# Kernel tuning notes

Measured on AMD Instinct MI355X. Metric: run time of the kernel, lower is better.

The kernel has to match this reference:

```python
import jax, jax.numpy as jnp
import numpy as np

B = 32
SEQ_LEN = 512      # T and n_fft
PRED_LEN = 96      # STFT window_size = PRED_LEN // 2 = 48
TOP_K = 3
D_MODEL = 512
D_FF = 512
N_HEADS = 8
C_OUT = 32         # graph node count
NODE_DIM = 10
CONV_CH = 32
SKIP_CH = 32
GCN_DEPTH = 2
PROP_ALPHA = 0.05
HOP = 48
EPS = 1e-5


def layer_norm(x, g, b):
    m = x.mean(-1, keepdims=True)
    v = ((x - m) ** 2).mean(-1, keepdims=True)
    return (x - m) * jax.lax.rsqrt(v + EPS) * g + b


def stft_mag(x):
    """torch.stft(center=True, hann window of len 48 center-padded to n_fft) magnitude,
    vmapped over channels. Returns [B, frames, n_fft//2+1, N]."""
    n_fft = SEQ_LEN
    win_len = PRED_LEN // 2
    n = jnp.arange(win_len, dtype=x.dtype)
    win = 0.5 - 0.5 * jnp.cos(2.0 * jnp.pi * n / win_len)   # periodic hann
    pad_l = (n_fft - win_len) // 2
    win = jnp.pad(win, (pad_l, n_fft - win_len - pad_l))     # center-pad window to n_fft
    T = x.shape[1]
    xp = jnp.pad(x, ((0, 0), (n_fft // 2, n_fft // 2), (0, 0)), mode='reflect')
    nfr = T // HOP + 1
    idx = jnp.arange(nfr)[:, None] * HOP + jnp.arange(n_fft)[None, :]
    frames = xp[:, idx, :]                                   # [B, nfr, n_fft, N]
    spec = jnp.fft.rfft(frames * win[None, None, :, None], axis=2)
    return jnp.abs(spec)


def attention_block(x, wq, bq, wk, bk, wv, bv, wo, bo, ff1_w, ff1_b, ff2_w, ff2_b,
                    n1_g, n1_b, n2_g, n2_b):
    M, S, D = x.shape
    H, Dh = N_HEADS, D // N_HEADS
    q = (x @ wq.T + bq).reshape(M, S, H, Dh)
    k = (x @ wk.T + bk).reshape(M, S, H, Dh)
    v = (x @ wv.T + bv).reshape(M, S, H, Dh)
    scores = jnp.einsum('mshd,mthd->mhst', q, k) * (1.0 / float(np.sqrt(Dh)))
    o = jnp.einsum('mhst,mthd->mshd', jax.nn.softmax(scores, axis=-1), v).reshape(M, S, D)
    x1 = layer_norm(x + (o @ wo.T + bo), n1_g, n1_b)
    y = jax.nn.gelu(x1 @ ff1_w.T + ff1_b, approximate=False) @ ff2_w.T + ff2_b
    return layer_norm(x1 + y, n2_g, n2_b)


def graph_block(x, nv1, nv2, sw, sb, mw, mb, ew, eb, lw, lb, g, b):
    # adaptive adjacency over C_OUT nodes
    adp = jax.nn.softmax(jax.nn.relu(nv1 @ nv2), axis=1)
    adj = adp + jnp.eye(C_OUT, dtype=x.dtype)
    a = adj / adj.sum(1, keepdims=True)
    # start_conv: [B,1,D,T] -> [B,CONV_CH,C_OUT,T]
    h = jax.lax.conv_general_dilated(x.transpose(0, 2, 1)[:, None], sw, (1, 1), 'VALID',
                                     dimension_numbers=('NCHW', 'OIHW', 'NCHW'))
    h = h + sb[None, :, None, None]
    x0, outs = h, [h]
    for _ in range(GCN_DEPTH):  # mixprop
        h = PROP_ALPHA * x0 + (1.0 - PROP_ALPHA) * jnp.einsum('bcwt,vw->bcvt', h, a)
        outs.append(h)
    ho = jnp.einsum('oc,bcnt->bont', mw, jnp.concatenate(outs, axis=1)) + mb[None, :, None, None]
    h = jax.nn.gelu(ho, approximate=False)
    out = jnp.einsum('bcns,tcs->btn', h, ew) + eb[None, :, None]   # end_conv (1,seq_len) kernel
    out = out @ lw + lb                                            # Linear c_out -> d_model
    return layer_norm(x + out, g, b)


def setup_inputs() -> dict:
    ks = jax.random.split(jax.random.key(0), 32)
    r = lambda i, shape, s=0.02: jax.random.normal(ks[i], shape, jnp.float32) * s
    kh = D_MODEL - C_OUT + 1
    return {
        'x': jax.random.normal(ks[0], (B, SEQ_LEN, D_MODEL), jnp.float32),
        'nv1': r(1, (TOP_K, C_OUT, NODE_DIM), 1.0),
        'nv2': r(2, (TOP_K, NODE_DIM, C_OUT), 1.0),
        'start_w': r(3, (TOP_K, CONV_CH, 1, kh, 1)),
        'start_b': r(4, (TOP_K, CONV_CH)),
        'mix_w': r(5, (TOP_K, SKIP_CH, (GCN_DEPTH + 1) * CONV_CH)),
        'mix_b': r(6, (TOP_K, SKIP_CH)),
        'end_w': r(7, (TOP_K, SEQ_LEN, SKIP_CH, SEQ_LEN)),
        'end_b': r(8, (TOP_K, SEQ_LEN)),
        'glin_w': r(9, (TOP_K, C_OUT, D_MODEL)),
        'glin_b': r(10, (TOP_K, D_MODEL)),
        'gnorm_g': 1.0 + r(11, (TOP_K, D_MODEL), 0.1),
        'gnorm_b': r(12, (TOP_K, D_MODEL), 0.1),
        'wq': r(13, (D_MODEL, D_MODEL)), 'bq': r(14, (D_MODEL,)),
        'wk': r(15, (D_MODEL, D_MODEL)), 'bk': r(16, (D_MODEL,)),
        'wv': r(17, (D_MODEL, D_MODEL)), 'bv': r(18, (D_MODEL,)),
        'wo': r(19, (D_MODEL, D_MODEL)), 'bo': r(20, (D_MODEL,)),
        'ff1_w': r(21, (D_FF, D_MODEL)), 'ff1_b': r(22, (D_FF,)),
        'ff2_w': r(23, (D_MODEL, D_FF)), 'ff2_b': r(24, (D_MODEL,)),
        'an1_g': 1.0 + r(25, (D_MODEL,), 0.1), 'an1_b': r(26, (D_MODEL,), 0.1),
        'an2_g': 1.0 + r(27, (D_MODEL,), 0.1), 'an2_b': r(28, (D_MODEL,), 0.1),
        'norm_g': 1.0 + r(29, (D_MODEL,), 0.1), 'norm_b': r(30, (D_MODEL,), 0.1),
    }


def reference(x, nv1, nv2, start_w, start_b, mix_w, mix_b, end_w, end_b, glin_w, glin_b,
              gnorm_g, gnorm_b, wq, bq, wk, bk, wv, bv, wo, bo,
              ff1_w, ff1_b, ff2_w, ff2_b, an1_g, an1_b, an2_g, an2_b, norm_g, norm_b):
    Bx, T, N = x.shape
    mag = stft_mag(x)                                   # [B, frames, Fbins, N]
    freq = mag.mean(axis=(0, 1, 3)).at[0].set(0.0)
    top = np.asarray(jax.lax.top_k(freq, TOP_K)[1])     # concrete: shapes below are data-dependent
    periods = [int(T // int(f)) for f in top]
    sw = jax.nn.softmax(mag[:, :, top, :].mean(axis=(1, 3)), axis=1)  # [B, k] scale weights
    cur = x
    res = []
    for i in range(TOP_K):
        scale = periods[i]
        # NOTE: faithful to the original bug: x is overwritten by gconv output each iteration
        cur = graph_block(cur, nv1[i], nv2[i], start_w[i], start_b[i], mix_w[i], mix_b[i],
                          end_w[i], end_b[i], glin_w[i], glin_b[i], gnorm_g[i], gnorm_b[i])
        length = -(-T // scale) * scale
        out = jnp.pad(cur, ((0, 0), (0, length - T), (0, 0))) if length > T else cur
        out = out.reshape(Bx * (length // scale), scale, N)
        out = attention_block(out, wq, bq, wk, bk, wv, bv, wo, bo,
                              ff1_w, ff1_b, ff2_w, ff2_b, an1_g, an1_b, an2_g, an2_b)
        out = jax.nn.gelu(layer_norm(out, norm_g, norm_b), approximate=False)
        out = out.reshape(Bx, length, N)[:, :T]
        res.append(out)
    res = jnp.stack(res, axis=-1)                       # [B, T, N, k]
    return (res * sw[:, None, None, :]).sum(-1) + cur
```

## Files before the change

### kernel.cpp

```cpp
#include <hip/hip_runtime.h>
#include <math.h>

#define DI __device__ __forceinline__

namespace {
constexpr int B_ = 32;
constexpr int T_ = 512;
constexpr int N_ = 512;
constexpr int C_ = 32;
constexpr int KH_ = 481;
constexpr int HOP_ = 48;
constexpr int WIN_ = 48;
constexpr int NFR_ = 11;
constexpr int NBIN_ = 257;
constexpr int NSB_ = 8 * NFR_ * B_;
constexpr int TOKMAX = 21760;
constexpr int PLW = TOKMAX * 512;
constexpr float EPS_ = 1e-5f;

constexpr size_t MBY = 1ull << 20;
constexpr size_t OFF_META = 0;
constexpr size_t OFF_FREQ = 4096;
constexpr size_t OFF_SW   = 8192;
constexpr size_t OFF_BEFF = 16384;
constexpr size_t OFF_P12  = 32768;
constexpr size_t OFF_FSB  = 65536;
constexpr size_t OFF_OSM  = 1 * MBY;
constexpr size_t OFF_WB   = 4 * MBY;
constexpr size_t OFF_WDH  = 10 * MBY;
constexpr size_t OFF_EWH  = 12 * MBY;
constexpr size_t OFF_CUR  = 44 * MBY;
constexpr size_t OFF_ACC  = 76 * MBY;
constexpr size_t TR       = 108 * MBY;
constexpr size_t OFF_T    = TR;
constexpr size_t OFF_WPH  = TR + 6 * MBY;
constexpr size_t OFF_G    = TR + 64 * MBY;
constexpr size_t OFF_G2   = TR + 128 * MBY;
constexpr size_t OFF_PART = TR + 192 * MBY;
constexpr size_t OFF_A0 = TR;
constexpr size_t OFF_A2 = TR + 44 * MBY;
constexpr size_t OFF_A3 = TR + 88 * MBY;
constexpr size_t OFF_A4 = TR + 132 * MBY;
constexpr size_t OFF_A5 = TR + 176 * MBY;
constexpr size_t OFF_FP = TR;
}

typedef __attribute__((ext_vector_type(2))) float f32x2;
typedef __attribute__((ext_vector_type(4))) float f32x4;
typedef __attribute__((ext_vector_type(8))) short bf8;
typedef __attribute__((ext_vector_type(8))) unsigned short u16x8;

DI float gelu_exact(float x) { return 0.5f * x * (1.0f + erff(x * 0.7071067811865475f)); }
DI unsigned short f2bf(float f) {
  unsigned u = __float_as_uint(f);
  u += 0x7FFFu + ((u >> 16) & 1u);
  return (unsigned short)(u >> 16);
}
DI float bf2f(unsigned short s) { return __uint_as_float(((unsigned)s) << 16); }
DI float ld2(const unsigned short* __restrict__ H, const unsigned short* __restrict__ L,
             size_t i) { return bf2f(H[i]) + bf2f(L[i]); }
DI void st2(unsigned short* __restrict__ H, unsigned short* __restrict__ L,
            size_t i, float v) {
  unsigned short h = f2bf(v);
  H[i] = h;
  L[i] = f2bf(v - bf2f(h));
}
DI void gll16(const unsigned short* g, unsigned short* l) {
  __builtin_amdgcn_global_load_lds(
      (const __attribute__((address_space(1))) void*)g,
      (__attribute__((address_space(3))) void*)l, 16, 0, 0);
}

__global__ __launch_bounds__(256) void k_stft2(const float* __restrict__ x,
                                               float* __restrict__ fpart) {
  int bid = blockIdx.x;
  int cc = bid & 7;
  int f = (bid >> 3) % NFR_;
  int b = bid / (8 * NFR_);
  __shared__ float xw[WIN_][64];
  int tid = threadIdx.x;
  for (int i = tid; i < WIN_ * 64; i += 256) {
    int j = i >> 6, n = i & 63;
    int gi = f * HOP_ + 232 + j - 256;
    if (gi < 0) gi = -gi;
    float w = 0.5f - 0.5f * cosf((float)j * 0.13089969389957472f);
    xw[j][n] = w * x[((size_t)b * T_ + gi) * N_ + cc * 64 + n];
  }
  __syncthreads();
  for (int pair = tid; pair < NBIN_ * 8; pair += 256) {
    int k = pair >> 3;
    int c4 = (pair & 7) * 4;
    int r0 = (k * 232) & 511;
    float a0 = (float)r0 * 0.012271846303085130f;
    float c = cosf(a0), s = sinf(a0);
    float dA = (float)k * 0.012271846303085130f;
    float cd = cosf(dA), sd = sinf(dA);
    f32x2 ri[8];
#pragma unroll
    for (int q = 0; q < 8; ++q) ri[q] = (f32x2){0.f, 0.f};
#pragma unroll 4
    for (int j = 0; j < WIN_; ++j) {
      float4 v0 = *(const float4*)&xw[j][c4];
      float4 v1 = *(const float4*)&xw[j][32 + c4];
      f32x2 cs = (f32x2){c, s};
      ri[0] += v0.x * cs;
      ri[1] += v0.y * cs;
      ri[2] += v0.z * cs;
      ri[3] += v0.w * cs;
      ri[4] += v1.x * cs;
      ri[5] += v1.y * cs;
      ri[6] += v1.z * cs;
      ri[7] += v1.w * cs;
      float cn = c * cd - s * sd;
      s = s * cd + c * sd;
      c = cn;
    }
    float m = 0.f;
#pragma unroll
    for (int q = 0; q < 8; ++q) m += sqrtf(ri[q].x * ri[q].x + ri[q].y * ri[q].y);
    for (int off = 4; off > 0; off >>= 1) m += __shfl_xor(m, off);
    if ((tid & 7) == 0) fpart[(size_t)k * NSB_ + bid] = m;
  }
}

__global__ __launch_bounds__(256) void k_fred(const float* __restrict__ fpart,
                                              float* __restrict__ freq,
                                              float* __restrict__ fsumb) {
  int k = blockIdx.x;
  int tid = threadIdx.x;
  int b = tid >> 3, j = tid & 7;
  float s = 0.f;
  for (int i = j; i < 88; i += 8) s += fpart[(size_t)k * NSB_ + b * 88 + i];
  for (int off = 4; off > 0; off >>= 1) s += __shfl_xor(s, off);
  __shared__ float bs[32];
  if (j == 0) bs[b] = s;
  __syncthreads();
  if (tid < 32) {
    float v = bs[tid];
    fsumb[k * 32 + tid] = v;
    for (int off = 16; off > 0; off >>= 1) v += __shfl_xor(v, off);
    if (tid == 0) freq[k] = v;
  }
}

__global__ void k_topk(const float* __restrict__ freq, const float* __restrict__ fsumb,
                       int* __restrict__ meta, float* __restrict__ swb) {
  __shared__ int stop[3];
  int tid = threadIdx.x;
  if (tid == 0) {
    float bv[3] = {-1e30f, -1e30f, -1e30f};
    int bi[3] = {1, 1, 1};
    for (int k = 1; k < NBIN_; ++k) {
      float v = freq[k];
      if (v > bv[0]) { bv[2]=bv[1]; bi[2]=bi[1]; bv[1]=bv[0]; bi[1]=bi[0]; bv[0]=v; bi[0]=k; }
      else if (v > bv[1]) { bv[2]=bv[1]; bi[2]=bi[1]; bv[1]=v; bi[1]=k; }
      else if (v > bv[2]) { bv[2]=v; bi[2]=k; }
    }
    for (int i = 0; i < 3; ++i) {
      int top = bi[i];
      int p = T_ / top;
      int L = ((T_ + p - 1) / p) * p;
      meta[i] = top;
      meta[3 + i] = p;
      meta[6 + i] = L;
      meta[9 + i] = L / p;
      meta[15 + i] = B_ * L;
      stop[i] = top;
    }
  }
  __syncthreads();
  int b = tid;
  if (b < B_) {
    float inv = 1.0f / (float)(NFR_ * N_);
    float m0 = fsumb[stop[0] * 32 + b] * inv;
    float m1 = fsumb[stop[1] * 32 + b] * inv;
    float m2 = fsumb[stop[2] * 32 + b] * inv;
    float mx = fmaxf(m0, fmaxf(m1, m2));
    float e0 = expf(m0 - mx), e1 = expf(m1 - mx), e2 = expf(m2 - mx);
    float s = e0 + e1 + e2;
    swb[b * 4 + 0] = e0 / s; swb[b * 4 + 1] = e1 / s; swb[b * 4 + 2] = e2 / s;
  }
}

__global__ __launch_bounds__(1024) void k_adjprep(const float* __restrict__ nv1,
                                                  const float* __restrict__ nv2,
                                                  const float* __restrict__ mw,
                                                  const float* __restrict__ mb,
                                                  const float* __restrict__ sb,
                                                  float* __restrict__ P12,
                                                  float* __restrict__ beff) {
  __shared__ float A32s[32][32];
  __shared__ float Ms[32][32], P1s[32][32], P2s[32][32], S1[32], S2[32], sbl[32];
  int tid = threadIdx.x;
  if (tid < 32) {
    int v = tid;
    float row[32];
    for (int w = 0; w < 32; ++w) {
      float s = 0.f;
      for (int d = 0; d < 10; ++d) s += nv1[v * 10 + d] * nv2[d * 32 + w];
      row[w] = fmaxf(s, 0.f);
    }
    float mx = -1e30f;
    for (int w = 0; w < 32; ++w) mx = fmaxf(mx, row[w]);
    float sm = 0.f;
    for (int w = 0; w < 32; ++w) { row[w] = expf(row[w] - mx); sm += row[w]; }
    for (int w = 0; w < 32; ++w) row[w] /= sm;
    row[v] += 1.0f;
    float rs = 0.f;
    for (int w = 0; w < 32; ++w) rs += row[w];
    for (int w = 0; w < 32; ++w) A32s[v][w] = row[w] / rs;
    sbl[tid] = sb[tid];
  }
  __syncthreads();
  int w = tid >> 5, v = tid & 31;
  Ms[w][v] = A32s[v][w];
  __syncthreads();
  float p1 = 0.95f * Ms[w][v] + (w == v ? 0.05f : 0.f);
  P1s[w][v] = p1;
  __syncthreads();
  float p2 = 0.f;
  for (int u = 0; u < 32; ++u) p2 += P1s[w][u] * Ms[u][v];
  p2 = 0.95f * p2 + (w == v ? 0.05f : 0.f);
  P2s[w][v] = p2;
  P12[tid] = p1;
  P12[1024 + tid] = p2;
  __syncthreads();
  if (tid < 32) {
    float s1 = 0.f, s2 = 0.f;
    for (int u = 0; u < 32; ++u) { s1 += P1s[u][tid]; s2 += P2s[u][tid]; }
    S1[tid] = s1; S2[tid] = s2;
  }
  __syncthreads();
  int o = w;
  float be = mb[o];
  for (int c = 0; c < 32; ++c) {
    float sc = sbl[c];
    be += mw[o * 96 + c] * sc;
    be += mw[o * 96 + 32 + c] * sc * S1[v];
    be += mw[o * 96 + 64 + c] * sc * S2[v];
  }
  beff[tid] = be;
}

__global__ __launch_bounds__(256) void k_T(const float* __restrict__ P12,
                                           const float* __restrict__ mw,
                                           float* __restrict__ Tm) {
  int idx = blockIdx.x * 256 + threadIdx.x;
  int r = idx >> 10, k2 = idx & 1023;
  int o = r >> 5, v = r & 31;
  int c = k2 >> 5, w = k2 & 31;
  float t = mw[o * 96 + 32 + c] * P12[w * 32 + v]
          + mw[o * 96 + 64 + c] * P12[1024 + w * 32 + v];
  if (w == v) t += mw[o * 96 + c];
  Tm[idx] = t;
}

__global__ void k_wdh(const float* __restrict__ swi, unsigned short* __restrict__ WH) {
  int idx = blockIdx.x * 256 + threadIdx.x;
  int j = idx >> 10, k2 = idx & 1023;
  int c = k2 >> 5, w = k2 & 31;
  int kk = j - w;
  float vv = (kk >= 0 && kk < KH_) ? swi[c * KH_ + kk] : 0.f;
  WH[idx] = f2bf(vv);
}

__global__ void k_splith(const float* __restrict__ src, unsigned short* __restrict__ Hi,
                         int n) {
  int i = blockIdx.x * 256 + threadIdx.x;
  if (i * 4 >= n) return;
  float4 v = *(const float4*)&src[i * 4];
  ushort4 h;
  h.x = f2bf(v.x); h.y = f2bf(v.y); h.z = f2bf(v.z); h.w = f2bf(v.w);
  *(ushort4*)&Hi[i * 4] = h;
}

__global__ __launch_bounds__(256, 2) void k_mm2(
    const float* __restrict__ A, const unsigned short* __restrict__ Bh,
    const float* __restrict__ bias,
    float* __restrict__ C, float* __restrict__ Cpart,
    int M, int N, int K, int lda, int dogelu) {
  const int bm = blockIdx.y * 128;
  if (bm >= M) return;
  const int bn = blockIdx.x * 128;
  const int nz = gridDim.z, z = blockIdx.z;
  const int kpb = K / nz;
  const int kbeg = z * kpb, kend = kbeg + kpb;

  __shared__ __align__(16) unsigned short AhS[4096], AlS[4096], BhS[4096];

  const int tid = threadIdx.x;
  const int wave = tid >> 6, lane = tid & 63;
  const int wr = wave >> 1, wc = wave & 1;
  const int fr = lane & 15, fs = lane >> 4;

  const int sr = tid >> 1, ss = (tid & 1) * 2;
  const int sx = (sr >> 1) & 3;
  const int so0 = sr * 32 + 8 * (ss ^ sx);
  const int so1 = sr * 32 + 8 * ((ss + 1) ^ sx);

  const int row0 = tid >> 2;
  const int s0 = (tid & 3) ^ ((row0 >> 1) & 3);
  const unsigned short* gBh0 = Bh + (size_t)(bn + row0) * K + s0 * 8;
  const unsigned short* gBh1 = gBh0 + (size_t)64 * K;
  unsigned short* lB0 = &BhS[wave * 512];
  unsigned short* lB1 = &BhS[2048 + wave * 512];

  int aoff[4], boff[4];
#pragma unroll
  for (int m = 0; m < 4; ++m) {
    int ra = wr * 64 + m * 16 + fr;
    aoff[m] = ra * 32 + 8 * (fs ^ ((ra >> 1) & 3));
    int rb = wc * 64 + m * 16 + fr;
    boff[m] = rb * 32 + 8 * (fs ^ ((rb >> 1) & 3));
  }

  const bool aok = (bm + sr) < M;
  const float* Arow = A + (size_t)(bm + sr) * lda + ss * 8;

  f32x4 acc[4][4];
#pragma unroll
  for (int m = 0; m < 4; ++m)
#pragma unroll
    for (int n = 0; n < 4; ++n) acc[m][n] = (f32x4){0.f, 0.f, 0.f, 0.f};

  for (int k0 = kbeg; k0 < kend; k0 += 32) {
    float4 a0, a1, a2, a3;
    if (aok) {
      const float4* p = (const float4*)(Arow + k0);
      a0 = p[0]; a1 = p[1]; a2 = p[2]; a3 = p[3];
    } else {
      a0 = a1 = a2 = a3 = make_float4(0.f, 0.f, 0.f, 0.f);
    }
    float av[16];
    av[0]=a0.x; av[1]=a0.y; av[2]=a0.z; av[3]=a0.w;
    av[4]=a1.x; av[5]=a1.y; av[6]=a1.z; av[7]=a1.w;
    av[8]=a2.x; av[9]=a2.y; av[10]=a2.z; av[11]=a2.w;
    av[12]=a3.x; av[13]=a3.y; av[14]=a3.z; av[15]=a3.w;
    u16x8 h0, h1, l0, l1;
#pragma unroll
    for (int j = 0; j < 8; ++j) {
      unsigned u = __float_as_uint(av[j]);
      h0[j] = (unsigned short)(u >> 16);
      float r2 = av[j] - __uint_as_float(u & 0xffff0000u);
      l0[j] = (unsigned short)(__float_as_uint(r2) >> 16);
      unsigned u2 = __float_as_uint(av[j + 8]);
      h1[j] = (unsigned short)(u2 >> 16);
      float r3 = av[j + 8] - __uint_as_float(u2 & 0xffff0000u);
      l1[j] = (unsigned short)(__float_as_uint(r3) >> 16);
    }
    __syncthreads();
    gll16(gBh0 + k0, lB0); gll16(gBh1 + k0, lB1);
    *(u16x8*)&AhS[so0] = h0; *(u16x8*)&AhS[so1] = h1;
    *(u16x8*)&AlS[so0] = l0; *(u16x8*)&AlS[so1] = l1;
    __syncthreads();
    bf8 ah[4], al4[4], bh4[4];
#pragma unroll
    for (int m = 0; m < 4; ++m) {
      ah[m]  = *(const bf8*)&AhS[aoff[m]];
      al4[m] = *(const bf8*)&AlS[aoff[m]];
    }
#pragma unroll
    for (int n = 0; n < 4; ++n) bh4[n] = *(const bf8*)&BhS[boff[n]];
#pragma unroll
    for (int m = 0; m < 4; ++m)
#pragma unroll
      for (int n = 0; n < 4; ++n) {
        acc[m][n] = __builtin_amdgcn_mfma_f32_16x16x32_bf16(ah[m],  bh4[n], acc[m][n], 0, 0, 0);
        acc[m][n] = __builtin_amdgcn_mfma_f32_16x16x32_bf16(al4[m], bh4[n], acc[m][n], 0, 0, 0);
      }
  }

  if (nz > 1) {
    float* P = Cpart + (size_t)z * M * N;
#pragma unroll
    for (int m = 0; m < 4; ++m)
#pragma unroll
      for (int r = 0; r < 4; ++r) {
        int row = bm + wr * 64 + m * 16 + fs * 4 + r;
        if (row < M) {
#pragma unroll
          for (int n = 0; n < 4; ++n) {
            int col = bn + wc * 64 + n * 16 + fr;
            P[(size_t)row * N + col] = acc[m][n][r];
          }
        }
      }
  } else {
    float bcol[4];
#pragma unroll
    for (int n = 0; n < 4; ++n) bcol[n] = bias ? bias[bn + wc * 64 + n * 16 + fr] : 0.f;
#pragma unroll
    for (int m = 0; m < 4; ++m)
#pragma unroll
      for (int r = 0; r < 4; ++r) {
        int row = bm + wr * 64 + m * 16 + fs * 4 + r;
        if (row < M) {
#pragma unroll
          for (int n = 0; n < 4; ++n) {
            int col = bn + wc * 64 + n * 16 + fr;
            float v = acc[m][n][r] + bcol[n];
            if (dogelu) v = gelu_exact(v);
            C[(size_t)row * N + col] = v;
          }
        }
      }
  }
}

__global__ __launch_bounds__(256, 4) void k_mmcv(
    const float* __restrict__ A, const unsigned short* __restrict__ Bh,
    const float* __restrict__ bias,
    unsigned short* __restrict__ C,
    int M, int N, int K, int lda) {
  const int bm = blockIdx.y * 128;
  const int bn = blockIdx.x * 128;

  __shared__ __align__(16) unsigned short AhS[4096], BhS[4096];

  const int tid = threadIdx.x;
  const int wave = tid >> 6, lane = tid & 63;
  const int wr = wave >> 1, wc = wave & 1;
  const int fr = lane & 15, fs = lane >> 4;

  const int sr = tid >> 1, ss = (tid & 1) * 2;
  const int sx = (sr >> 1) & 3;
  const int so0 = sr * 32 + 8 * (ss ^ sx);
  const int so1 = sr * 32 + 8 * ((ss + 1) ^ sx);

  const int row0 = tid >> 2;
  const int s0 = (tid & 3) ^ ((row0 >> 1) & 3);
  const unsigned short* gBh0 = Bh + (size_t)(bn + row0) * K + s0 * 8;
  const unsigned short* gBh1 = gBh0 + (size_t)64 * K;
  unsigned short* lB0 = &BhS[wave * 512];
  unsigned short* lB1 = &BhS[2048 + wave * 512];

// ... 411 lines not shown
  __syncthreads();
  float d0 = val[0] - mean, d1 = val[1] - mean;
  red[tid] = d0 * d0 + d1 * d1;
  __syncthreads();
  for (int off = 128; off > 0; off >>= 1) { if (tid < off) red[tid] += red[tid + off]; __syncthreads(); }
  float inv = rsqrtf(red[0] * (1.0f / N_) + EPS_);
  st2(dh, dl, (size_t)tok * N_ + tid, d0 * inv * g[tid] + bt[tid]);
  st2(dh, dl, (size_t)tok * N_ + tid + 256, d1 * inv * g[tid + 256] + bt[tid + 256]);
}

__global__ __launch_bounds__(256) void k_lnfin(const unsigned short* __restrict__ r1h,
                                               const unsigned short* __restrict__ r1l,
                                               const unsigned short* __restrict__ r2h,
                                               const unsigned short* __restrict__ r2l,
                                               const float* __restrict__ g1,
                                               const float* __restrict__ b1,
                                               const float* __restrict__ g2,
                                               const float* __restrict__ b2,
                                               const float* __restrict__ swb,
                                               float* __restrict__ acc,
                                               const int* __restrict__ meta, int iter) {
  int L = meta[6 + iter];
  int tok = blockIdx.x;
  if (tok >= B_ * L) return;
  int b = tok / L, l = tok % L;
  if (l >= T_) return;
  __shared__ float red[256];
  int tid = threadIdx.x;
  float val[2];
#pragma unroll
  for (int q = 0; q < 2; ++q) {
    size_t i = (size_t)tok * N_ + tid + q * 256;
    val[q] = ld2(r1h, r1l, i) + ld2(r2h, r2l, i);
  }
  red[tid] = val[0] + val[1];
  __syncthreads();
  for (int off = 128; off > 0; off >>= 1) { if (tid < off) red[tid] += red[tid + off]; __syncthreads(); }
  float mean = red[0] * (1.0f / N_);
  __syncthreads();
  float d0 = val[0] - mean, d1 = val[1] - mean;
  red[tid] = d0 * d0 + d1 * d1;
  __syncthreads();
  for (int off = 128; off > 0; off >>= 1) { if (tid < off) red[tid] += red[tid + off]; __syncthreads(); }
  float inv = rsqrtf(red[0] * (1.0f / N_) + EPS_);
  float y0 = d0 * inv * g1[tid] + b1[tid];
  float y1 = d1 * inv * g1[tid + 256] + b1[tid + 256];
  __syncthreads();
  red[tid] = y0 + y1;
  __syncthreads();
  for (int off = 128; off > 0; off >>= 1) { if (tid < off) red[tid] += red[tid + off]; __syncthreads(); }
  float mean2 = red[0] * (1.0f / N_);
  __syncthreads();
  float e0 = y0 - mean2, e1 = y1 - mean2;
  red[tid] = e0 * e0 + e1 * e1;
  __syncthreads();
  for (int off = 128; off > 0; off >>= 1) { if (tid < off) red[tid] += red[tid + off]; __syncthreads(); }
  float inv2 = rsqrtf(red[0] * (1.0f / N_) + EPS_);
  float s = swb[b * 4 + iter];
  float u0 = gelu_exact(e0 * inv2 * g2[tid] + b2[tid]);
  float u1 = gelu_exact(e1 * inv2 * g2[tid + 256] + b2[tid + 256]);
  size_t o = ((size_t)b * T_ + l) * N_;
  acc[o + tid] += s * u0;
  acc[o + tid + 256] += s * u1;
}

__global__ __launch_bounds__(256) void k_attn32(
    const unsigned short* __restrict__ qh,
    const unsigned short* __restrict__ kh,
    const unsigned short* __restrict__ vh,
    unsigned short* __restrict__ oh,
    const int* __restrict__ meta, int iter) {
  int S = meta[3 + iter];
  if (S > 32) return;
  int L = meta[6 + iter], nseq = meta[9 + iter];
  int npair = B_ * nseq * 8;
  __shared__ float Kt[4][64 * 33];
  __shared__ unsigned short Vsh[4][32 * 66];
  __shared__ float qs[4][64];
  int tid = threadIdx.x;
  int wave = tid >> 6, lane = tid & 63;
  float* Ktw = Kt[wave];
  unsigned short* Vw = Vsh[wave];
  int gw = (blockIdx.x * 256 + tid) >> 6;
  int nw = (gridDim.x * 256) >> 6;
  const int tt = lane & 31;
  const int hf = lane >> 5;
  for (int pair = gw; pair < npair; pair += nw) {
    int h = pair & 7;
    int m = pair >> 3;
    int b = m / nseq, g2 = m - b * nseq;
    size_t base = ((size_t)b * L + (size_t)g2 * S) * N_ + h * 64;
    for (int i = lane; i < S * 64; i += 64) {
      int t = i >> 6, d = i & 63;
      size_t gi = base + (size_t)t * N_ + d;
      Ktw[d * 33 + t] = bf2f(kh[gi]);
      Vw[t * 66 + d] = vh[gi];
    }
    bool tok = tt < S;
    for (int s = 0; s < S; ++s) {
      qs[wave][lane] = bf2f(qh[base + (size_t)s * N_ + lane]);
      float part = 0.f;
      if (tok) {
        const float* kp = &Ktw[hf * 32 * 33 + tt];
        const float* qp = &qs[wave][hf * 32];
#pragma unroll 8
        for (int j = 0; j < 32; ++j) part += qp[j] * kp[j * 33];
      }
      part += __shfl_xor(part, 32);
      float sc = tok ? part * 0.125f : -3.0e38f;
      float mx = sc;
      for (int off = 16; off > 0; off >>= 1) mx = fmaxf(mx, __shfl_xor(mx, off));
      float p = tok ? expf(sc - mx) : 0.f;
      float ssum = p;
      for (int off = 16; off > 0; off >>= 1) ssum += __shfl_xor(ssum, off);
      float ov = 0.f;
      for (int t = 0; t < S; ++t) {
        float pt = __shfl(p, t);
        ov += pt * bf2f(Vw[t * 66 + lane]);
      }
      oh[base + (size_t)s * N_ + lane] = f2bf(ov / ssum);
    }
  }
}

__global__ __launch_bounds__(512) void k_attn_small(
    const unsigned short* __restrict__ qh,
    const unsigned short* __restrict__ kh,
    const unsigned short* __restrict__ vh,
    unsigned short* __restrict__ oh,
    const int* __restrict__ meta, int iter) {
  int S = meta[3 + iter];
  if (S <= 32 || S > 128) return;
  int L = meta[6 + iter], nseq = meta[9 + iter];
  int M = B_ * nseq;
  int mh = blockIdx.x;
  int m = mh >> 3, h = mh & 7;
  if (m >= M) return;
  int b = m / nseq, g2 = m % nseq;
  size_t tok0 = (size_t)b * L + (size_t)g2 * S;
  __shared__ float Ks[64 * 129];
  __shared__ float Vs[128 * 65];
  __shared__ float qrow[8][64];
  __shared__ float Pr[8][128];
  int tid = threadIdx.x;
  for (int i = tid; i < S * 64; i += 512) {
    int t = i >> 6, d = i & 63;
    size_t gi = (tok0 + t) * N_ + h * 64 + d;
    Ks[d * 129 + t] = bf2f(kh[gi]);
    Vs[t * 65 + d] = bf2f(vh[gi]);
  }
  __syncthreads();
  int wave = tid >> 6, lane = tid & 63;
  for (int s = wave; s < S; s += 8) {
    qrow[wave][lane] = bf2f(qh[(tok0 + s) * N_ + h * 64 + lane]);
    float sc0 = -3.0e38f, sc1 = -3.0e38f;
    if (lane < S) {
      float ad = 0.f;
#pragma unroll 16
      for (int j = 0; j < 64; ++j) ad += qrow[wave][j] * Ks[j * 129 + lane];
      sc0 = ad * 0.125f;
    }
    if (S > 64 && lane + 64 < S) {
      float ad = 0.f;
#pragma unroll 16
      for (int j = 0; j < 64; ++j) ad += qrow[wave][j] * Ks[j * 129 + lane + 64];
      sc1 = ad * 0.125f;
    }
    float mx = fmaxf(sc0, sc1);
    for (int off = 32; off > 0; off >>= 1) mx = fmaxf(mx, __shfl_xor(mx, off));
    float e0 = (lane < S) ? expf(sc0 - mx) : 0.f;
    float e1 = (S > 64 && lane + 64 < S) ? expf(sc1 - mx) : 0.f;
    if (lane < S) Pr[wave][lane] = e0;
    if (S > 64 && lane + 64 < S) Pr[wave][lane + 64] = e1;
    float ssum = e0 + e1;
    for (int off = 32; off > 0; off >>= 1) ssum += __shfl_xor(ssum, off);
    float ov = 0.f;
#pragma unroll 8
    for (int t = 0; t < S; ++t) ov += Pr[wave][t] * Vs[t * 65 + lane];
    oh[(tok0 + s) * N_ + h * 64 + lane] = f2bf(ov / ssum);
  }
}

__global__ __launch_bounds__(256) void k_attn_big(
    const unsigned short* __restrict__ qh,
    const unsigned short* __restrict__ kh,
    const unsigned short* __restrict__ vh,
    unsigned short* __restrict__ oh,
    const int* __restrict__ meta, int iter) {
  int p = meta[3 + iter];
  if (p <= 128) return;
  int L = meta[6 + iter], nseq = meta[9 + iter];
  int M = B_ * nseq;
  int mh = blockIdx.x;
  int m = mh >> 3, h = mh & 7;
  if (m >= M) return;
  int S = p;
  int b = m / nseq, g2 = m % nseq;
  size_t tok0 = (size_t)b * L + (size_t)g2 * S;
  __shared__ unsigned short Ks[512 * 66];
  __shared__ unsigned short Vs[512 * 66];
  __shared__ float qrow[4][64];
  __shared__ float Pr[4][512];
  int tid = threadIdx.x;
  for (int i = tid; i < S * 64; i += 256) {
    int t = i >> 6, d = i & 63;
    size_t gi = (tok0 + t) * N_ + h * 64 + d;
    Ks[t * 66 + d] = kh[gi];
    Vs[t * 66 + d] = vh[gi];
  }
  __syncthreads();
  int wave = tid >> 6, lane = tid & 63;
  for (int s = wave; s < S; s += 4) {
    qrow[wave][lane] = bf2f(qh[(tok0 + s) * N_ + h * 64 + lane]);
    const float2* qp = (const float2*)&qrow[wave][0];
    float sc[8];
    float mx = -3.0e38f;
#pragma unroll
    for (int c2 = 0; c2 < 8; ++c2) {
      int t = lane + c2 * 64;
      float sv = -3.0e38f;
      if (t < S) {
        const unsigned int* kp = (const unsigned int*)&Ks[t * 66];
        float ad = 0.f;
#pragma unroll
        for (int j2 = 0; j2 < 32; ++j2) {
          float2 qq = qp[j2];
          unsigned int kw = kp[j2];
          ad += qq.x * bf2f((unsigned short)(kw & 0xffffu));
          ad += qq.y * bf2f((unsigned short)(kw >> 16));
        }
        sv = ad * 0.125f;
      }
      sc[c2] = sv;
      mx = fmaxf(mx, sv);
    }
    for (int off = 32; off > 0; off >>= 1) mx = fmaxf(mx, __shfl_xor(mx, off));
    float ssum = 0.f;
#pragma unroll
    for (int c2 = 0; c2 < 8; ++c2) {
      int t = lane + c2 * 64;
      float e = 0.f;
      if (t < S) { e = expf(sc[c2] - mx); Pr[wave][t] = e; }
      ssum += e;
    }
    for (int off = 32; off > 0; off >>= 1) ssum += __shfl_xor(ssum, off);
    float inv = 1.0f / ssum;
    float ov = 0.f;
#pragma unroll 8
    for (int t = 0; t < S; ++t) ov += Pr[wave][t] * bf2f(Vs[t * 66 + lane]);
    oh[(tok0 + s) * N_ + h * 64 + lane] = f2bf(ov * inv);
  }
}

__global__ void k_final(const float* __restrict__ acc, const float* __restrict__ cur,
                        float* __restrict__ out) {
  size_t idx = (size_t)blockIdx.x * 256 + threadIdx.x;
  out[idx] = acc[idx] + cur[idx];
}

extern "C" void kernel_launch(void* const* d_in, const int* in_sizes, int n_in,
                              void* d_out, int out_size, void* d_ws, size_t ws_size,
                              hipStream_t stream) {
  (void)in_sizes; (void)n_in; (void)out_size; (void)ws_size;
  const float* x       = (const float*)d_in[0];
  const float* nv1     = (const float*)d_in[1];
  const float* nv2     = (const float*)d_in[2];
  const float* start_w = (const float*)d_in[3];
  const float* start_b = (const float*)d_in[4];
  const float* mix_w   = (const float*)d_in[5];
  const float* mix_b   = (const float*)d_in[6];
  const float* end_w   = (const float*)d_in[7];
  const float* end_b   = (const float*)d_in[8];
  const float* glin_w  = (const float*)d_in[9];
  const float* glin_b  = (const float*)d_in[10];
  const float* gnorm_g = (const float*)d_in[11];
  const float* gnorm_b = (const float*)d_in[12];
  const float* wq = (const float*)d_in[13];
  const float* bq = (const float*)d_in[14];
  const float* wk = (const float*)d_in[15];
  const float* bk = (const float*)d_in[16];
  const float* wv = (const float*)d_in[17];
  const float* bv = (const float*)d_in[18];
  const float* wo = (const float*)d_in[19];
  const float* bo = (const float*)d_in[20];
  const float* ff1w = (const float*)d_in[21];
  const float* ff1b = (const float*)d_in[22];
  const float* ff2w = (const float*)d_in[23];
  const float* ff2b = (const float*)d_in[24];
  const float* an1g = (const float*)d_in[25];
  const float* an1b = (const float*)d_in[26];
  const float* an2g = (const float*)d_in[27];
  const float* an2b = (const float*)d_in[28];
  const float* nrmg = (const float*)d_in[29];
  const float* nrmb = (const float*)d_in[30];

  char* ws = (char*)d_ws;
  int*   meta = (int*)(ws + OFF_META);
  float* freq = (float*)(ws + OFF_FREQ);
  float* swb  = (float*)(ws + OFF_SW);
  float* beff = (float*)(ws + OFF_BEFF);
  float* P12  = (float*)(ws + OFF_P12);
  float* fsumb = (float*)(ws + OFF_FSB);
  float* osm  = (float*)(ws + OFF_OSM);
  unsigned short* WB  = (unsigned short*)(ws + OFF_WB);
  unsigned short* WdH = (unsigned short*)(ws + OFF_WDH);
  unsigned short* EWH = (unsigned short*)(ws + OFF_EWH);
  float* cur  = (float*)(ws + OFF_CUR);
  float* accb = (float*)(ws + OFF_ACC);
  float* fpart = (float*)(ws + OFF_FP);
  float* Tm   = (float*)(ws + OFF_T);
  unsigned short* WPH = (unsigned short*)(ws + OFF_WPH);
  unsigned short* Gb  = (unsigned short*)(ws + OFF_G);
  unsigned short* G2b = (unsigned short*)(ws + OFF_G2);
  float* PART = (float*)(ws + OFF_PART);
  unsigned short* A0h = (unsigned short*)(ws + OFF_A0); unsigned short* A0l = A0h + PLW;
  unsigned short* A2h = (unsigned short*)(ws + OFF_A2); unsigned short* A2l = A2h + PLW;
  unsigned short* A3h = (unsigned short*)(ws + OFF_A3); unsigned short* A3l = A3h + PLW;
  unsigned short* A4h = (unsigned short*)(ws + OFF_A4);
  unsigned short* A5h = (unsigned short*)(ws + OFF_A5); unsigned short* A5l = A5h + PLW;

  hipMemsetAsync(accb, 0, (size_t)B_ * T_ * N_ * 4, stream);

  k_stft2<<<NSB_, 256, 0, stream>>>(x, fpart);
  k_fred<<<NBIN_, 256, 0, stream>>>(fpart, freq, fsumb);
  k_topk<<<1, 64, 0, stream>>>(freq, fsumb, meta, swb);

  const float* wlist[6] = {wq, wk, wv, wo, ff1w, ff2w};
  for (int w = 0; w < 6; ++w)
    k_splith<<<256, 256, 0, stream>>>(wlist[w], WB + (size_t)w * 262144, 262144);
  unsigned short* WqkvH = WB;
  unsigned short* WoH = WB + 3 * 262144;
  unsigned short* F1H = WB + 4 * 262144;
  unsigned short* F2H = WB + 5 * 262144;

  const float* curIn = x;
  for (int i = 0; i < 3; ++i) {
    k_adjprep<<<1, 1024, 0, stream>>>(nv1 + i * C_ * 10, nv2 + i * 10 * C_,
                                      mix_w + i * C_ * 96, mix_b + i * C_,
                                      start_b + i * C_, P12, beff);
    k_T<<<4096, 256, 0, stream>>>(P12, mix_w + i * C_ * 96, Tm);
    k_wdh<<<2048, 256, 0, stream>>>(start_w + i * C_ * KH_, WdH);
    k_mm2<<<dim3(4, 8, 8), 256, 0, stream>>>(Tm, WdH, nullptr, nullptr, PART,
                                             1024, 512, 1024, 1024, 0);
    k_redsplit<<<2048, 256, 0, stream>>>(PART, WPH);
    k_mmcv<<<dim3(8, 128), 256, 0, stream>>>(curIn, WPH, beff, Gb, 16384, 1024, 512, 512);
    k_repackb<<<B_ * C_ * 16, 256, 0, stream>>>(Gb, G2b);
    k_splith<<<8192, 256, 0, stream>>>(end_w + (size_t)i * 8388608, EWH, 8388608);
    k_mmend<<<dim3(4, 8, 16), 256, 0, stream>>>(G2b, EWH, PART, 1024, 512, 16384);
    k_red16<<<2048, 256, 0, stream>>>(PART, end_b + i * T_, osm);
    k_lwln<<<B_ * T_, 256, 0, stream>>>(osm, glin_w + i * C_ * N_, glin_b + i * N_, curIn,
                                        gnorm_g + i * N_, gnorm_b + i * N_, cur,
                                        A0h, A0l, meta, i);
    k_padtail<<<512, 256, 0, stream>>>(A0h, A0l, meta, i);
    const int* Mdyn = meta + 15 + i;
    dim3 gT(4, TOKMAX / 128, 1);
    k_mmqkv<<<dim3(12, TOKMAX / 128), 256, 0, stream>>>(A0h, WqkvH, bq, bk, bv,
                                                        A2h, A3h, A4h, TOKMAX, 512, Mdyn);
    k_attn32<<<2048, 256, 0, stream>>>(A2h, A3h, A4h, A5h, meta, i);
    k_attn_small<<<4096, 512, 0, stream>>>(A2h, A3h, A4h, A5h, meta, i);
    k_attn_big<<<1024, 256, 0, stream>>>(A2h, A3h, A4h, A5h, meta, i);
    k_mmb1<<<gT, 256, 0, stream>>>(A5h, WoH, bo, A2h, A2l, TOKMAX, 512, 512, Mdyn, 0);
    k_lnadd<<<TOKMAX, 256, 0, stream>>>(A0h, A0l, A2h, A2l, an1g, an1b, A3h, A3l, meta, i);
    k_mmb1<<<gT, 256, 0, stream>>>(A3h, F1H, ff1b, A4h, nullptr, TOKMAX, 512, 512, Mdyn, 1);
    k_mmb1<<<gT, 256, 0, stream>>>(A4h, F2H, ff2b, A5h, A5l, TOKMAX, 512, 512, Mdyn, 0);
    k_lnfin<<<TOKMAX, 256, 0, stream>>>(A3h, A3l, A5h, A5l, an2g, an2b, nrmg, nrmb,
                                        swb, accb, meta, i);
    curIn = cur;
  }
  k_final<<<(B_ * T_ * N_) / 256, 256, 0, stream>>>(accb, curIn, (float*)d_out);
}
```

Measured before the change: 2.016 ms.

## Recast STFT magnitude as split-bf16 MFMA GEMM against precomputed twiddles

```diff
diff --git a/kernel.cpp b/kernel.cpp
--- a/kernel.cpp
+++ b/kernel.cpp
@@ -13,7 +13,7 @@
 constexpr int WIN_ = 48;
 constexpr int NFR_ = 11;
 constexpr int NBIN_ = 257;
-constexpr int NSB_ = 8 * NFR_ * B_;
+constexpr int NMT_ = B_ * NFR_ * 4;
 constexpr int TOKMAX = 21760;
 constexpr int PLW = TOKMAX * 512;
 constexpr float EPS_ = 1e-5f;
@@ -26,6 +26,8 @@
 constexpr size_t OFF_P12  = 32768;
 constexpr size_t OFF_FSB  = 65536;
 constexpr size_t OFF_OSM  = 1 * MBY;
+constexpr size_t OFF_TWH  = 3 * MBY;
+constexpr size_t OFF_TWL  = 3 * MBY + 131072;
 constexpr size_t OFF_WB   = 4 * MBY;
 constexpr size_t OFF_WDH  = 10 * MBY;
 constexpr size_t OFF_EWH  = 12 * MBY;
@@ -42,7 +44,9 @@
 constexpr size_t OFF_A3 = TR + 88 * MBY;
 constexpr size_t OFF_A4 = TR + 132 * MBY;
 constexpr size_t OFF_A5 = TR + 176 * MBY;
-constexpr size_t OFF_FP = TR;
+constexpr size_t OFF_XWH = TR;
+constexpr size_t OFF_XWL = TR + 24 * MBY;
+constexpr size_t OFF_FP  = TR + 48 * MBY;
 }
 
 typedef __attribute__((ext_vector_type(2))) float f32x2;
@@ -71,55 +75,160 @@
       (__attribute__((address_space(3))) void*)l, 16, 0, 0);
 }
 
-__global__ __launch_bounds__(256) void k_stft2(const float* __restrict__ x,
-                                               float* __restrict__ fpart) {
-  int bid = blockIdx.x;
-  int cc = bid & 7;
-  int f = (bid >> 3) % NFR_;
-  int b = bid / (8 * NFR_);
-  __shared__ float xw[WIN_][64];
+__global__ __launch_bounds__(256) void k_xw(const float* __restrict__ x,
+                                            unsigned short* __restrict__ XWH,
+                                            unsigned short* __restrict__ XWL) {
+  int bf = blockIdx.x;
+  int f = bf % NFR_, b = bf / NFR_;
   int tid = threadIdx.x;
-  for (int i = tid; i < WIN_ * 64; i += 256) {
-    int j = i >> 6, n = i & 63;
-    int gi = f * HOP_ + 232 + j - 256;
-    if (gi < 0) gi = -gi;
+  for (int i = tid; i < 512 * 8; i += 256) {
+    int n = i >> 3, jc = i & 7;
+    size_t m = (size_t)bf * 512 + n;
+    u16x8 vh, vl;
+#pragma unroll
+    for (int q = 0; q < 8; ++q) {
+      int j = jc * 8 + q;
+      if (j < WIN_) {
+        int gi = f * HOP_ + 232 + j - 256;
+        if (gi < 0) gi = -gi;
+        float v = x[((size_t)b * T_ + gi) * N_ + n];
+        unsigned short h = f2bf(v);
+        vh[q] = h;
+        vl[q] = f2bf(v - bf2f(h));
+      } else { vh[q] = 0; vl[q] = 0; }
+    }
+    *(u16x8*)&XWH[m * 64 + jc * 8] = vh;
+    *(u16x8*)&XWL[m * 64 + jc * 8] = vl;
+  }
+}
+
+__global__ void k_tw(unsigned short* __restrict__ TWH, unsigned short* __restrict__ TWL) {
+  int idx = blockIdx.x * 256 + threadIdx.x;
+  if (idx >= 2 * 384 * 64) return;
+  int pl = idx / (384 * 64);
+  int rem = idx % (384 * 64);
+  int k = rem >> 6, j = rem & 63;
+  float v = 0.f;
+  if (k < NBIN_ && j < WIN_) {
+    int r = (k * (232 + j)) & 511;
+    float ang = (float)r * 0.012271846303085130f;
     float w = 0.5f - 0.5f * cosf((float)j * 0.13089969389957472f);
-    xw[j][n] = w * x[((size_t)b * T_ + gi) * N_ + cc * 64 + n];
-  }
-  __syncthreads();
-  for (int pair = tid; pair < NBIN_ * 8; pair += 256) {
-    int k = pair >> 3;
-    int c4 = (pair & 7) * 4;
-    int r0 = (k * 232) & 511;
-    float a0 = (float)r0 * 0.012271846303085130f;
-    float c = cosf(a0), s = sinf(a0);
-    float dA = (float)k * 0.012271846303085130f;
-    float cd = cosf(dA), sd = sinf(dA);
-    f32x2 ri[8];
-#pragma unroll
-    for (int q = 0; q < 8; ++q) ri[q] = (f32x2){0.f, 0.f};
-#pragma unroll 4
-    for (int j = 0; j < WIN_; ++j) {
-      float4 v0 = *(const float4*)&xw[j][c4];
-      float4 v1 = *(const float4*)&xw[j][32 + c4];
-      f32x2 cs = (f32x2){c, s};
-      ri[0] += v0.x * cs;
-      ri[1] += v0.y * cs;
-      ri[2] += v0.z * cs;
-      ri[3] += v0.w * cs;
-      ri[4] += v1.x * cs;
-      ri[5] += v1.y * cs;
-      ri[6] += v1.z * cs;
-      ri[7] += v1.w * cs;
-      float cn = c * cd - s * sd;
-      s = s * cd + c * sd;
-      c = cn;
-    }
-    float m = 0.f;
-#pragma unroll
-    for (int q = 0; q < 8; ++q) m += sqrtf(ri[q].x * ri[q].x + ri[q].y * ri[q].y);
-    for (int off = 4; off > 0; off >>= 1) m += __shfl_xor(m, off);
-    if ((tid & 7) == 0) fpart[(size_t)k * NSB_ + bid] = m;
+    v = pl == 0 ? w * cosf(ang) : w * sinf(ang);
+  }
+  unsigned short h = f2bf(v);
+  TWH[idx] = h;
+  TWL[idx] = f2bf(v - bf2f(h));
+}
+
+__global__ __launch_bounds__(256, 2) void k_stftmm(
+    const unsigned short* __restrict__ XWH, const unsigned short* __restrict__ XWL,
+    const unsigned short* __restrict__ TWH, const unsigned short* __restrict__ TWL,
+    float* __restrict__ fpart) {
+  const int bn = blockIdx.x * 128;
+  const int mtile = blockIdx.y;
+  const int bm = mtile * 128;
+
+  __shared__ __align__(16) unsigned short AHS[4096], ALS[4096], RHS[4096], RLS[4096],
+                                          IHS[4096], ILS[4096];
+  __shared__ float colpart[2][128];
+
+  const int tid = threadIdx.x;
+  const int wave = tid >> 6, lane = tid & 63;
+  const int wr = wave >> 1, wc = wave & 1;
+  const int fr = lane & 15, fs = lane >> 4;
+
+  const int row0 = tid >> 2;
+  const int s0 = (tid & 3) ^ ((row0 >> 1) & 3);
+  const unsigned short* gAH0 = XWH + (size_t)(bm + row0) * 64 + s0 * 8;
+  const unsigned short* gAH1 = gAH0 + (size_t)64 * 64;
+  const unsigned short* gAL0 = XWL + (size_t)(bm + row0) * 64 + s0 * 8;
+  const unsigned short* gAL1 = gAL0 + (size_t)64 * 64;
+  const unsigned short* gRH0 = TWH + (size_t)(bn + row0) * 64 + s0 * 8;
+  const unsigned short* gRH1 = gRH0 + (size_t)64 * 64;
+  const unsigned short* gRL0 = TWL + (size_t)(bn + row0) * 64 + s0 * 8;
+  const unsigned short* gRL1 = gRL0 + (size_t)64 * 64;
+  const unsigned short* gIH0 = gRH0 + (size_t)384 * 64;
+  const unsigned short* gIH1 = gRH1 + (size_t)384 * 64;
+  const unsigned short* gIL0 = gRL0 + (size_t)384 * 64;
+  const unsigned short* gIL1 = gRL1 + (size_t)384 * 64;
+  const int lb0 = wave * 512, lb1 = 2048 + wave * 512;
+
+  int aoff[4], boff[4];
+#pragma unroll
+  for (int m = 0; m < 4; ++m) {
+    int ra = wr * 64 + m * 16 + fr;
+    aoff[m] = ra * 32 + 8 * (fs ^ ((ra >> 1) & 3));
+    int rb = wc * 64 + m * 16 + fr;
+    boff[m] = rb * 32 + 8 * (fs ^ ((rb >> 1) & 3));
+  }
+
+  f32x4 are[4][4], aim[4][4];
+#pragma unroll
+  for (int m = 0; m < 4; ++m)
+#pragma unroll
+    for (int n = 0; n < 4; ++n) {
+      are[m][n] = (f32x4){0.f, 0.f, 0.f, 0.f};
+      aim[m][n] = (f32x4){0.f, 0.f, 0.f, 0.f};
+    }
+
+  for (int k0 = 0; k0 < 64; k0 += 32) {
+    __syncthreads();
+    gll16(gAH0 + k0, &AHS[lb0]); gll16(gAH1 + k0, &AHS[lb1]);
+    gll16(gAL0 + k0, &ALS[lb0]); gll16(gAL1 + k0, &ALS[lb1]);
+    gll16(gRH0 + k0, &RHS[lb0]); gll16(gRH1 + k0, &RHS[lb1]);
+    gll16(gRL0 + k0, &RLS[lb0]); gll16(gRL1 + k0, &RLS[lb1]);
+    gll16(gIH0 + k0, &IHS[lb0]); gll16(gIH1 + k0, &IHS[lb1]);
+    gll16(gIL0 + k0, &ILS[lb0]); gll16(gIL1 + k0, &ILS[lb1]);
+    __syncthreads();
+    bf8 ah[4], al[4], rh[4], rl[4], ih[4], il[4];
+#pragma unroll
+    for (int m = 0; m < 4; ++m) {
+      ah[m] = *(const bf8*)&AHS[aoff[m]];
+      al[m] = *(const bf8*)&ALS[aoff[m]];
+    }
+#pragma unroll
+    for (int n = 0; n < 4; ++n) {
+      rh[n] = *(const bf8*)&RHS[boff[n]];
+      rl[n] = *(const bf8*)&RLS[boff[n]];
+      ih[n] = *(const bf8*)&IHS[boff[n]];
+      il[n] = *(const bf8*)&ILS[boff[n]];
+    }
+#pragma unroll
+    for (int m = 0; m < 4; ++m)
+#pragma unroll
+      for (int n = 0; n < 4; ++n) {
+        are[m][n] = __builtin_amdgcn_mfma_f32_16x16x32_bf16(ah[m], rh[n], are[m][n], 0, 0, 0);
+        are[m][n] = __builtin_amdgcn_mfma_f32_16x16x32_bf16(ah[m], rl[n], are[m][n], 0, 0, 0);
+        are[m][n] = __builtin_amdgcn_mfma_f32_16x16x32_bf16(al[m], rh[n], are[m][n], 0, 0, 0);
+        aim[m][n] = __builtin_amdgcn_mfma_f32_16x16x32_bf16(ah[m], ih[n], aim[m][n], 0, 0, 0);
+        aim[m][n] = __builtin_amdgcn_mfma_f32_16x16x32_bf16(ah[m], il[n], aim[m][n], 0, 0, 0);
+        aim[m][n] = __builtin_amdgcn_mfma_f32_16x16x32_bf16(al[m], ih[n], aim[m][n], 0, 0, 0);
+      }
+  }
+
+  float s[4];
+#pragma unroll
+  for (int n = 0; n < 4; ++n) {
+    float acc = 0.f;
+#pragma unroll
+    for (int m = 0; m < 4; ++m)
+#pragma unroll
+      for (int r = 0; r < 4; ++r) {
+        float re = are[m][n][r], im = aim[m][n][r];
+        acc += sqrtf(re * re + im * im);
+      }
+    acc += __shfl_xor(acc, 16);
+    acc += __shfl_xor(acc, 32);
+    s[n] = acc;
+  }
+  if (fs == 0) {
+#pragma unroll
+    for (int n = 0; n < 4; ++n) colpart[wr][wc * 64 + n * 16 + fr] = s[n];
+  }
+  __syncthreads();
+  if (tid < 128) {
+    int k = bn + tid;
+    if (k < NBIN_) fpart[(size_t)k * NMT_ + mtile] = colpart[0][tid] + colpart[1][tid];
   }
 }
 
@@ -130,7 +239,7 @@
   int tid = threadIdx.x;
   int b = tid >> 3, j = tid & 7;
   float s = 0.f;
-  for (int i = j; i < 88; i += 8) s += fpart[(size_t)k * NSB_ + b * 88 + i];
+  for (int i = j; i < 44; i += 8) s += fpart[(size_t)k * NMT_ + b * 44 + i];
   for (int off = 4; off > 0; off >>= 1) s += __shfl_xor(s, off);
   __shared__ float bs[32];
   if (j == 0) bs[b] = s;
@@ -1148,11 +1257,15 @@
   float* P12  = (float*)(ws + OFF_P12);
   float* fsumb = (float*)(ws + OFF_FSB);
   float* osm  = (float*)(ws + OFF_OSM);
+  unsigned short* TWH = (unsigned short*)(ws + OFF_TWH);
+  unsigned short* TWL = (unsigned short*)(ws + OFF_TWL);
   unsigned short* WB  = (unsigned short*)(ws + OFF_WB);
   unsigned short* WdH = (unsigned short*)(ws + OFF_WDH);
   unsigned short* EWH = (unsigned short*)(ws + OFF_EWH);
   float* cur  = (float*)(ws + OFF_CUR);
   float* accb = (float*)(ws + OFF_ACC);
+  unsigned short* XWH = (unsigned short*)(ws + OFF_XWH);
+  unsigned short* XWL = (unsigned short*)(ws + OFF_XWL);
   float* fpart = (float*)(ws + OFF_FP);
   float* Tm   = (float*)(ws + OFF_T);
   unsigned short* WPH = (unsigned short*)(ws + OFF_WPH);
@@ -1167,7 +1280,9 @@
 
   hipMemsetAsync(accb, 0, (size_t)B_ * T_ * N_ * 4, stream);
 
-  k_stft2<<<NSB_, 256, 0, stream>>>(x, fpart);
+  k_xw<<<B_ * NFR_, 256, 0, stream>>>(x, XWH, XWL);
+  k_tw<<<(2 * 384 * 64 + 255) / 256, 256, 0, stream>>>(TWH, TWL);
+  k_stftmm<<<dim3(3, NMT_), 256, 0, stream>>>(XWH, XWL, TWH, TWL, fpart);
   k_fred<<<NBIN_, 256, 0, stream>>>(fpart, freq, fsumb);
   k_topk<<<1, 64, 0, stream>>>(freq, fsumb, meta, swb);
 
```

Measured after the change: 2.020 ms. About the same (+0.2%).
